# Kernel optimization log

Hardware: AMD Instinct MI355X
Metric: run time of the kernel (lower is better)

Reference implementation:

```python
import jax, jax.numpy as jnp
import numpy as np

N = 100000      # nodes
E = 1600000     # edges (avg degree 16)
H = 128         # hidden_dim
V = 64          # vector_dim
NUM_LAYERS = 3


def setup_inputs() -> dict:
    key = jax.random.key(0)
    ks = jax.random.split(key, 16)
    s = 0.05
    inp = {
        "node_feats": jax.random.normal(ks[0], (N, 1), dtype=jnp.float32),
        "edge_index": jax.random.randint(ks[1], (2, E), 0, N, dtype=jnp.int64),
        "batch": jnp.zeros((N,), dtype=jnp.int64),
        "temperature": jnp.float32(1.0),
        "t": jnp.float32(1.0),
        # SAGEConv layer 0: in=1 -> out=H. PyG: lin_l (on aggregated, with bias), lin_r (on root, no bias)
        "Wl0": jax.random.normal(ks[2], (1, H), dtype=jnp.float32) * s,
        "bl0": jnp.zeros((H,), dtype=jnp.float32),
        "Wr0": jax.random.normal(ks[3], (1, H), dtype=jnp.float32) * s,
        # SAGEConv layers 1..2: H -> H, stacked
        "Wl": jax.random.normal(ks[4], (NUM_LAYERS - 1, H, H), dtype=jnp.float32) * s,
        "bl": jnp.zeros((NUM_LAYERS - 1, H), dtype=jnp.float32),
        "Wr": jax.random.normal(ks[5], (NUM_LAYERS - 1, H, H), dtype=jnp.float32) * s,
        # to_vector: H -> V
        "Wv": jax.random.normal(ks[6], (H, V), dtype=jnp.float32) * s,
        "bv": jnp.zeros((V,), dtype=jnp.float32),
        # mlp: (V+2) -> H -> 1
        "Wm1": jax.random.normal(ks[7], (V + 2, H), dtype=jnp.float32) * s,
        "bm1": jnp.zeros((H,), dtype=jnp.float32),
        "Wm2": jax.random.normal(ks[8], (H, 1), dtype=jnp.float32) * s,
        "bm2": jnp.zeros((1,), dtype=jnp.float32),
    }
    return inp


def reference(node_feats, edge_index, batch, temperature, t,
              Wl0, bl0, Wr0, Wl, bl, Wr, Wv, bv, Wm1, bm1, Wm2, bm2):
    n = node_feats.shape[0]
    src, dst = edge_index[0], edge_index[1]
    # in-degree for scatter-mean (clamp to 1 for isolated nodes, like PyG mean aggr)
    deg = jax.ops.segment_sum(jnp.ones((src.shape[0],), node_feats.dtype), dst, num_segments=n)
    deg = jnp.maximum(deg, 1.0)[:, None]  # (N,1)

    def sage(h, Wl_, bl_, Wr_):
        # scatter-mean of source features onto destination nodes
        agg = jax.ops.segment_sum(h[src], dst, num_segments=n) / deg
        return agg @ Wl_ + bl_ + h @ Wr_

    h = node_feats.reshape(-1, 1)  # (N,1)
    h = jax.nn.relu(sage(h, Wl0, bl0, Wr0))
    for i in range(Wl.shape[0]):
        h = jax.nn.relu(sage(h, Wl[i], bl[i], Wr[i]))

    # global_mean_pool over single graph (batch all zeros)
    num_graphs = 1
    cnt = jax.ops.segment_sum(jnp.ones((n,), h.dtype), batch, num_segments=num_graphs)
    pooled = jax.ops.segment_sum(h, batch, num_segments=num_graphs) / jnp.maximum(cnt, 1.0)[:, None]  # (1,H)

    z = pooled @ Wv + bv  # (1,V)  (no ReLU in original code path)
    extras = jnp.stack([jnp.asarray(temperature, z.dtype), jnp.asarray(t, z.dtype)]).reshape(1, 2)
    feat = jnp.concatenate([z, extras], axis=1)  # (1, V+2)
    out = jax.nn.softplus(jax.nn.relu(feat @ Wm1 + bm1) @ Wm2 + bm2)  # (1,1)
    return out
```

## Files before the change

### kernel.cpp

```cpp
#include <hip/hip_runtime.h>
#include <hip/hip_bf16.h>
#include <math.h>

#define H 128
#define BKT_SHIFT 9
#define BKT_NODES 512
#define CHUNK 2048
#define GEMM_GRID 512
#define FP8_SCALE 64.0f
#define FP8_INV (1.0f / 64.0f)

typedef __attribute__((ext_vector_type(8))) short short8;
typedef __attribute__((ext_vector_type(4))) float f32x4;
typedef __attribute__((ext_vector_type(2))) float f32x2;

static __device__ __forceinline__ ushort f2b(float v) {
    union { float f; unsigned u; } x; x.f = v;
    unsigned r = x.u + 0x7fffu + ((x.u >> 16) & 1u);
    return (ushort)(r >> 16);
}
static __device__ __forceinline__ float b2f(ushort b) {
    union { unsigned u; float f; } x; x.u = ((unsigned)b) << 16;
    return x.f;
}


__global__ void bucket_hist_kernel(const int* __restrict__ dst, int e,
                                   int* __restrict__ bucketCount, int* __restrict__ blockBase) {
    __shared__ int hist[256];
    int t = threadIdx.x;
    hist[t] = 0;
    __syncthreads();
    int base = blockIdx.x * CHUNK;
    #pragma unroll
    for (int k = 0; k < CHUNK / 256; k++) {
        int i = base + k * 256 + t;
        if (i < e) atomicAdd(&hist[dst[i] >> BKT_SHIFT], 1);
    }
    __syncthreads();
    blockBase[blockIdx.x * 256 + t] = atomicAdd(&bucketCount[t], hist[t]);
}

__global__ void bucket_scan_kernel(const int* __restrict__ bucketCount, int* __restrict__ bucketBase,
                                   int* __restrict__ rs, int n, int e) {
    if (threadIdx.x == 0 && blockIdx.x == 0) {
        int acc = 0;
        for (int i = 0; i < 256; i++) { bucketBase[i] = acc; acc += bucketCount[i]; }
        bucketBase[256] = acc;
        rs[n] = e;
    }
}

__global__ void bucket_scatter_kernel(const int* __restrict__ src, const int* __restrict__ dst, int e,
                                      const int* __restrict__ bucketBase, const int* __restrict__ blockBase,
                                      int2* __restrict__ grouped) {
    __shared__ int cur[256];
    int t = threadIdx.x;
    cur[t] = bucketBase[t] + blockBase[blockIdx.x * 256 + t];
    __syncthreads();
    int base = blockIdx.x * CHUNK;
    #pragma unroll
    for (int k = 0; k < CHUNK / 256; k++) {
        int i = base + k * 256 + t;
        if (i < e) {
            int d = dst[i];
            int pos = atomicAdd(&cur[d >> BKT_SHIFT], 1);
            int2 p; p.x = d; p.y = src[i];
            grouped[pos] = p;
        }
    }
}

__global__ void bucket_csr_kernel(const int2* __restrict__ grouped, const int* __restrict__ bucketBase,
                                  int* __restrict__ rs, int* __restrict__ csr, int n) {
    __shared__ int sdeg[BKT_NODES];
    __shared__ int sexcl[BKT_NODES];
    __shared__ int wsum[4];
    int b = blockIdx.x;
    int t = threadIdx.x;
    int nodeBase = b << BKT_SHIFT;
    int ebase = bucketBase[b], eend = bucketBase[b + 1];
    sdeg[t] = 0; sdeg[t + 256] = 0;
    __syncthreads();
    for (int e = ebase + t; e < eend; e += 256)
        atomicAdd(&sdeg[grouped[e].x - nodeBase], 1);
    __syncthreads();
    int lane = t & 63, wid = t >> 6;
    int v0 = sdeg[2 * t], v1 = sdeg[2 * t + 1];
    int p = v0 + v1;
    int x = p;
    #pragma unroll
    for (int off = 1; off < 64; off <<= 1) {
        int y = __shfl_up(x, off, 64);
        if (lane >= off) x += y;
    }
    if (lane == 63) wsum[wid] = x;
    __syncthreads();
    if (t == 0) {
        int acc = 0;
        #pragma unroll
        for (int w = 0; w < 4; w++) { int tmp = wsum[w]; wsum[w] = acc; acc += tmp; }
    }
    __syncthreads();
    int basep = wsum[wid] + x - p;
    sexcl[2 * t] = basep;
    sexcl[2 * t + 1] = basep + v0;
    int nodes = min(BKT_NODES, n - nodeBase);
    for (int i = t; i < nodes; i += 256) rs[nodeBase + i] = ebase + sexcl[i];
    sdeg[t] = 0; sdeg[t + 256] = 0;
    __syncthreads();
    for (int e = ebase + t; e < eend; e += 256) {
        int2 pr = grouped[e];
        int l = pr.x - nodeBase;
        int r = atomicAdd(&sdeg[l], 1);
        csr[ebase + sexcl[l] + r] = pr.y;
    }
}


__global__ void prep_w_kernel(const float* __restrict__ Wl, const float* __restrict__ Wr,
                              ushort* __restrict__ Btg) {
    int idx = blockIdx.x * 256 + threadIdx.x;
    if (idx >= 65536) return;
    int l = idx >> 15;
    int col = (idx >> 8) & 127;
    int k = idx & 255;
    float v = (k < 128) ? Wl[l * H * H + k * H + col] : Wr[l * H * H + (k - 128) * H + col];
    Btg[idx] = f2b(v);
}


__global__ void agg0_kernel(const float* __restrict__ x, const int* __restrict__ rs,
                            const int* __restrict__ csr, float* __restrict__ agg0, int n) {
    int i = blockIdx.x * 256 + threadIdx.x;
    if (i >= n) return;
    int a = rs[i], b = rs[i + 1];
    float s = 0.f;
    for (int e = a; e < b; e++) s += x[csr[e]];
    agg0[i] = s / (float)max(b - a, 1);
}

__global__ void expand0_kernel(const float* __restrict__ x, const float* __restrict__ agg0,
                               const float* __restrict__ Wl0, const float* __restrict__ bl0,
                               const float* __restrict__ Wr0, ushort* __restrict__ hout,
                               ushort* __restrict__ h8, int n) {
    int idx = blockIdx.x * 256 + threadIdx.x;
    if (idx >= n * 64) return;
    int i = idx >> 6, j = (idx & 63) * 2;
    float gi = agg0[i], xi = x[i];
    float v0 = fmaxf(gi * Wl0[j] + bl0[j] + xi * Wr0[j], 0.f);
    float v1 = fmaxf(gi * Wl0[j + 1] + bl0[j + 1] + xi * Wr0[j + 1], 0.f);
    ushort2 o; o.x = f2b(v0); o.y = f2b(v1);
    *(ushort2*)(hout + (size_t)i * H + j) = o;
    int p = __builtin_amdgcn_cvt_pk_fp8_f32(v0 * FP8_SCALE, v1 * FP8_SCALE, 0, false);
    h8[(size_t)i * 64 + (idx & 63)] = (ushort)p;
}


__global__ void aggregate8_kernel(const unsigned char* __restrict__ h8, const int* __restrict__ rs,
                                  const int* __restrict__ csr, ushort* __restrict__ aggb, int n) {
    int tid = threadIdx.x;
    int w = (tid >> 5) & 1;
    int node = blockIdx.x * 8 + (tid >> 6) * 2 + w;
    if (node >= n) return;
    int sl = (tid >> 3) & 3;
    int fl = tid & 7;
    int a = rs[node], b = rs[node + 1];
    f32x2 s[8];
    #pragma unroll
    for (int j = 0; j < 8; j++) s[j] = (f32x2){0.f, 0.f};

    int e = a;
    for (; e + 8 <= b; e += 8) {
        int n0 = csr[e + sl], n1 = csr[e + 4 + sl];
        uint4 u0 = *(const uint4*)(h8 + (size_t)n0 * 128 + 16 * fl);
        uint4 u1 = *(const uint4*)(h8 + (size_t)n1 * 128 + 16 * fl);
        unsigned dw[8] = {u0.x, u0.y, u0.z, u0.w, u1.x, u1.y, u1.z, u1.w};
        #pragma unroll
        for (int d = 0; d < 8; d++) {
            f32x2 lo = __builtin_amdgcn_cvt_pk_f32_fp8(dw[d], false);
            f32x2 hi = __builtin_amdgcn_cvt_pk_f32_fp8(dw[d], true);
            s[(d & 3) * 2] += lo;
            s[(d & 3) * 2 + 1] += hi;
        }
    }
    for (; e + 4 <= b; e += 4) {
        int n0 = csr[e + sl];
        uint4 u0 = *(const uint4*)(h8 + (size_t)n0 * 128 + 16 * fl);
        unsigned dw[4] = {u0.x, u0.y, u0.z, u0.w};
        #pragma unroll
        for (int d = 0; d < 4; d++) {
            f32x2 lo = __builtin_amdgcn_cvt_pk_f32_fp8(dw[d], false);
            f32x2 hi = __builtin_amdgcn_cvt_pk_f32_fp8(dw[d], true);
            s[d * 2] += lo;
            s[d * 2 + 1] += hi;
        }
    }
    if (e < b && sl < (b - e)) {
        int n0 = csr[e + sl];
        uint4 u0 = *(const uint4*)(h8 + (size_t)n0 * 128 + 16 * fl);
        unsigned dw[4] = {u0.x, u0.y, u0.z, u0.w};
        #pragma unroll
        for (int d = 0; d < 4; d++) {
            f32x2 lo = __builtin_amdgcn_cvt_pk_f32_fp8(dw[d], false);
            f32x2 hi = __builtin_amdgcn_cvt_pk_f32_fp8(dw[d], true);
            s[d * 2] += lo;
            s[d * 2 + 1] += hi;
        }
    }
    #pragma unroll
    for (int j = 0; j < 8; j++) {
        s[j].x += __shfl_xor(s[j].x, 8, 64);
        s[j].y += __shfl_xor(s[j].y, 8, 64);
        s[j].x += __shfl_xor(s[j].x, 16, 64);
        s[j].y += __shfl_xor(s[j].y, 16, 64);
    }
    if (sl == 0) {
        float inv = FP8_INV / (float)max(b - a, 1);
        short8 o0, o1;
        #pragma unroll
        for (int j = 0; j < 4; j++) {
            o0[2 * j]     = (short)f2b(s[j].x * inv);
            o0[2 * j + 1] = (short)f2b(s[j].y * inv);
            o1[2 * j]     = (short)f2b(s[j + 4].x * inv);
            o1[2 * j + 1] = (short)f2b(s[j + 4].y * inv);
        }
        ushort* dstp = aggb + (size_t)node * H + 16 * fl;
        *(short8*)dstp = o0;
        *(short8*)(dstp + 8) = o1;
    }
}


template<bool POOL>
__global__ __launch_bounds__(256, 2) void gemm_kernel(
    const ushort* __restrict__ aggb, const ushort* __restrict__ hb,
    const ushort* __restrict__ Btg,
    const float* __restrict__ bias, ushort* __restrict__ out,
    unsigned char* __restrict__ out8,
    float* __restrict__ partial, int nblk, int n) {
    __shared__ float sums[2][128];
    int tid = threadIdx.x;
    int wave = tid >> 6, lane = tid & 63;
    int l15 = lane & 15, lhi = lane >> 4;
    int colhalf = wave & 1;
    int rowsub = wave >> 1;
    int colbase = colhalf * 64;

    short8 bf[4][8];
    #pragma unroll
    for (int c2 = 0; c2 < 4; c2++) {
        const ushort* wp = Btg + (colbase + c2 * 16 + l15) * 256 + lhi * 8;
        #pragma unroll
        for (int s = 0; s < 8; s++)
            bf[c2][s] = *(const short8*)(wp + s * 32);
    }
    f32x4 bias_v[4];
    #pragma unroll
    for (int c2 = 0; c2 < 4; c2++)
        bias_v[c2] = *(const f32x4*)(bias + colbase + c2 * 16 + lhi * 4);

    f32x4 fs[4];
    #pragma unroll
    for (int c2 = 0; c2 < 4; c2++) fs[c2] = (f32x4){0.f, 0.f, 0.f, 0.f};

    for (int r0 = blockIdx.x * 32; r0 < n; r0 += nblk * 32) {
        int row = r0 + rowsub * 16 + l15;
        int arow = min(row, n - 1);
        short8 af[8];
        #pragma unroll
        for (int s = 0; s < 8; s++)
            af[s] = *(const short8*)((s < 4 ? aggb : hb) + (size_t)arow * H + (s & 3) * 32 + lhi * 8);
        f32x4 acc[4];
        #pragma unroll
        for (int c2 = 0; c2 < 4; c2++) acc[c2] = (f32x4){0.f, 0.f, 0.f, 0.f};
        #pragma unroll
        for (int s = 0; s < 8; s++) {
            #pragma unroll
            for (int c2 = 0; c2 < 4; c2++)
                acc[c2] = __builtin_amdgcn_mfma_f32_16x16x32_bf16(bf[c2][s], af[s], acc[c2], 0, 0, 0);
        }
        if (row < n) {
            if (POOL) {
                #pragma unroll
                for (int c2 = 0; c2 < 4; c2++)
                    #pragma unroll
                    for (int r = 0; r < 4; r++)
                        fs[c2][r] += fmaxf(acc[c2][r] + bias_v[c2][r], 0.f);
            } else {
                #pragma unroll
                for (int c2 = 0; c2 < 4; c2++) {
                    float v0 = fmaxf(acc[c2][0] + bias_v[c2][0], 0.f);
                    float v1 = fmaxf(acc[c2][1] + bias_v[c2][1], 0.f);
                    float v2 = fmaxf(acc[c2][2] + bias_v[c2][2], 0.f);
                    float v3 = fmaxf(acc[c2][3] + bias_v[c2][3], 0.f);
                    ushort4 o;
                    o.x = f2b(v0); o.y = f2b(v1); o.z = f2b(v2); o.w = f2b(v3);
                    *(ushort4*)(out + (size_t)row * H + colbase + c2 * 16 + lhi * 4) = o;
                    int p = __builtin_amdgcn_cvt_pk_fp8_f32(v0 * FP8_SCALE, v1 * FP8_SCALE, 0, false);
                    p = __builtin_amdgcn_cvt_pk_fp8_f32(v2 * FP8_SCALE, v3 * FP8_SCALE, p, true);
                    *(unsigned int*)(out8 + (size_t)row * 128 + colbase + c2 * 16 + lhi * 4) = (unsigned)p;
                }
            }
        }
    }

    if (POOL) {
        #pragma unroll
        for (int c2 = 0; c2 < 4; c2++) {
            #pragma unroll
            for (int m = 1; m < 16; m <<= 1) {
                #pragma unroll
                for (int r = 0; r < 4; r++)
                    fs[c2][r] += __shfl_xor(fs[c2][r], m, 64);
            }
        }
        if (l15 == 0) {
            #pragma unroll
            for (int c2 = 0; c2 < 4; c2++)
                #pragma unroll
                for (int r = 0; r < 4; r++)
                    sums[rowsub][colbase + c2 * 16 + lhi * 4 + r] = fs[c2][r];
        }
        __syncthreads();
        if (tid < 128)
            partial[tid * nblk + blockIdx.x] = sums[0][tid] + sums[1][tid];
    }
}


__global__ void pool_reduce_kernel(const float* __restrict__ partial, float* __restrict__ pooled,
                                   int nb, float invn) {
    int j = blockIdx.x;
    int t = threadIdx.x;
    float s = 0.f;
    for (int b = t; b < nb; b += 64) s += partial[j * nb + b];
    #pragma unroll
    for (int off = 32; off > 0; off >>= 1) s += __shfl_down(s, off, 64);
    if (t == 0) pooled[j] = s * invn;
}


__global__ void mlp_kernel(const float* __restrict__ pooled,
                           const float* __restrict__ Wv, const float* __restrict__ bv,
                           const float* __restrict__ temp, const float* __restrict__ tt,
                           const float* __restrict__ Wm1, const float* __restrict__ bm1,
                           const float* __restrict__ Wm2, const float* __restrict__ bm2,
                           float* __restrict__ out) {
    __shared__ float feat[66];
    __shared__ float red[2];
    int j = threadIdx.x;
    if (j < 64) {
        float s = bv[j];
        for (int k = 0; k < H; k++) s += pooled[k] * Wv[k * 64 + j];
        feat[j] = s;
    }
    if (j == 64) feat[64] = temp[0];
    if (j == 65) feat[65] = tt[0];
    __syncthreads();
    float m = bm1[j];
    for (int k = 0; k < 66; k++) m += feat[k] * Wm1[k * H + j];
    m = fmaxf(m, 0.f);
    float p = m * Wm2[j];
    #pragma unroll
    for (int off = 32; off > 0; off >>= 1) p += __shfl_down(p, off, 64);
    if ((j & 63) == 0) red[j >> 6] = p;
    __syncthreads();
    if (j == 0) {
        float x = red[0] + red[1] + bm2[0];
        out[0] = (x > 20.f) ? x : log1pf(expf(x));
    }
}


extern "C" void kernel_launch(void* const* d_in, const int* in_sizes, int n_in,
                              void* d_out, int out_size, void* d_ws, size_t ws_size,
                              hipStream_t stream) {
    const float* node_feats = (const float*)d_in[0];
    const int* edge_index = (const int*)d_in[1];
    const float* temp = (const float*)d_in[3];
    const float* tt   = (const float*)d_in[4];
    const float* Wl0 = (const float*)d_in[5];
    const float* bl0 = (const float*)d_in[6];
    const float* Wr0 = (const float*)d_in[7];
    const float* Wl  = (const float*)d_in[8];
    const float* bl  = (const float*)d_in[9];
    const float* Wr  = (const float*)d_in[10];
    const float* Wv  = (const float*)d_in[11];
    const float* bv  = (const float*)d_in[12];
    const float* Wm1 = (const float*)d_in[13];
    const float* bm1 = (const float*)d_in[14];
    const float* Wm2 = (const float*)d_in[15];
    const float* bm2 = (const float*)d_in[16];

    const int N = in_sizes[0];
    const int E = in_sizes[1] / 2;
    const int* src = edge_index;
    const int* dst = edge_index + E;

    size_t NH = (size_t)N * H;
    ushort* hA   = (ushort*)d_ws;
    ushort* hB   = hA + NH;
    ushort* aggb = hB + NH;
    ushort* Btg  = aggb + NH;
    float* agg0  = (float*)(Btg + 65536);
    int2* grouped = (int2*)(agg0 + N);
    int* csr     = (int*)(grouped + E);
    int* rs      = csr + E;
    int* bucketCount = rs + (N + 1);
    int* bucketBase  = bucketCount + 256;
    int* blockBase   = bucketBase + 257;
    int NBLK = (E + CHUNK - 1) / CHUNK;
    float* partial = (float*)(blockBase + NBLK * 256);
    float* pooled  = partial + (size_t)H * GEMM_GRID;
    unsigned char* hB8 = (unsigned char*)(pooled + H);
    unsigned char* hA8 = (unsigned char*)grouped;

    int NB = (N + BKT_NODES - 1) / BKT_NODES;

    hipMemsetAsync(bucketCount, 0, 256 * sizeof(int), stream);
    bucket_hist_kernel<<<NBLK, 256, 0, stream>>>(dst, E, bucketCount, blockBase);
    bucket_scan_kernel<<<1, 64, 0, stream>>>(bucketCount, bucketBase, rs, N, E);
    bucket_scatter_kernel<<<NBLK, 256, 0, stream>>>(src, dst, E, bucketBase, blockBase, grouped);
    bucket_csr_kernel<<<NB, 256, 0, stream>>>(grouped, bucketBase, rs, csr, N);

    prep_w_kernel<<<256, 256, 0, stream>>>(Wl, Wr, Btg);

    agg0_kernel<<<(N + 255) / 256, 256, 0, stream>>>(node_feats, rs, csr, agg0, N);
    expand0_kernel<<<((size_t)N * 64 + 255) / 256, 256, 0, stream>>>(
        node_feats, agg0, Wl0, bl0, Wr0, hA, (ushort*)hA8, N);

    aggregate8_kernel<<<(N + 7) / 8, 256, 0, stream>>>(hA8, rs, csr, aggb, N);
    gemm_kernel<false><<<GEMM_GRID, 256, 0, stream>>>(aggb, hA, Btg, bl, hB, hB8, nullptr, GEMM_GRID, N);

    aggregate8_kernel<<<(N + 7) / 8, 256, 0, stream>>>(hB8, rs, csr, aggb, N);
    gemm_kernel<true><<<GEMM_GRID, 256, 0, stream>>>(aggb, hB, Btg + 32768, bl + H, nullptr, nullptr, partial, GEMM_GRID, N);

    pool_reduce_kernel<<<H, 64, 0, stream>>>(partial, pooled, GEMM_GRID, 1.0f / (float)N);
    mlp_kernel<<<1, H, 0, stream>>>(pooled, Wv, bv, temp, tt, Wm1, bm1, Wm2, bm2, (float*)d_out);
}
```

Measured before the change: 259.4 us.

## Drop bf16 node features, use fp8 root input in GEMM, fuse layer0 and pool/MLP

The bf16 copies of the hidden states are removed. The GEMM now reads the root features from the fp8 buffer, converts them to bf16 in registers, and folds the fp8 scale into Wr. Bucket scatter packs (src<<9 | local dst) into one 32-bit word instead of an int2, halving that traffic. agg0 and expand0 merge into a single layer0 kernel with vectorized fp8 stores, and pool_reduce plus mlp merge into one kernel. Root features now lose precision to fp8, and the packing assumes node indices fit in 23 bits.

```diff
diff --git a/kernel.cpp b/kernel.cpp
--- a/kernel.cpp
+++ b/kernel.cpp
@@ -19,10 +19,6 @@
     unsigned r = x.u + 0x7fffu + ((x.u >> 16) & 1u);
     return (ushort)(r >> 16);
 }
-static __device__ __forceinline__ float b2f(ushort b) {
-    union { unsigned u; float f; } x; x.u = ((unsigned)b) << 16;
-    return x.f;
-}
 
 
 __global__ void bucket_hist_kernel(const int* __restrict__ dst, int e,
@@ -53,7 +49,7 @@
 
 __global__ void bucket_scatter_kernel(const int* __restrict__ src, const int* __restrict__ dst, int e,
                                       const int* __restrict__ bucketBase, const int* __restrict__ blockBase,
-                                      int2* __restrict__ grouped) {
+                                      unsigned* __restrict__ grouped) {
     __shared__ int cur[256];
     int t = threadIdx.x;
     cur[t] = bucketBase[t] + blockBase[blockIdx.x * 256 + t];
@@ -65,13 +61,12 @@
         if (i < e) {
             int d = dst[i];
             int pos = atomicAdd(&cur[d >> BKT_SHIFT], 1);
-            int2 p; p.x = d; p.y = src[i];
-            grouped[pos] = p;
-        }
-    }
-}
-
-__global__ void bucket_csr_kernel(const int2* __restrict__ grouped, const int* __restrict__ bucketBase,
+            grouped[pos] = ((unsigned)src[i] << 9) | (unsigned)(d & 511);
+        }
+    }
+}
+
+__global__ void bucket_csr_kernel(const unsigned* __restrict__ grouped, const int* __restrict__ bucketBase,
                                   int* __restrict__ rs, int* __restrict__ csr, int n) {
     __shared__ int sdeg[BKT_NODES];
     __shared__ int sexcl[BKT_NODES];
@@ -83,7 +78,7 @@
     sdeg[t] = 0; sdeg[t + 256] = 0;
     __syncthreads();
     for (int e = ebase + t; e < eend; e += 256)
-        atomicAdd(&sdeg[grouped[e].x - nodeBase], 1);
+        atomicAdd(&sdeg[grouped[e] & 511u], 1);
     __syncthreads();
     int lane = t & 63, wid = t >> 6;
     int v0 = sdeg[2 * t], v1 = sdeg[2 * t + 1];
@@ -110,10 +105,10 @@
     sdeg[t] = 0; sdeg[t + 256] = 0;
     __syncthreads();
     for (int e = ebase + t; e < eend; e += 256) {
-        int2 pr = grouped[e];
-        int l = pr.x - nodeBase;
+        unsigned pr = grouped[e];
+        int l = (int)(pr & 511u);
         int r = atomicAdd(&sdeg[l], 1);
-        csr[ebase + sexcl[l] + r] = pr.y;
+        csr[ebase + sexcl[l] + r] = (int)(pr >> 9);
     }
 }
 
@@ -125,35 +120,57 @@
     int l = idx >> 15;
     int col = (idx >> 8) & 127;
     int k = idx & 255;
-    float v = (k < 128) ? Wl[l * H * H + k * H + col] : Wr[l * H * H + (k - 128) * H + col];
+    float v = (k < 128) ? Wl[l * H * H + k * H + col]
+                        : Wr[l * H * H + (k - 128) * H + col] * FP8_INV;
     Btg[idx] = f2b(v);
 }
 
 
-__global__ void agg0_kernel(const float* __restrict__ x, const int* __restrict__ rs,
-                            const int* __restrict__ csr, float* __restrict__ agg0, int n) {
-    int i = blockIdx.x * 256 + threadIdx.x;
-    if (i >= n) return;
-    int a = rs[i], b = rs[i + 1];
-    float s = 0.f;
-    for (int e = a; e < b; e++) s += x[csr[e]];
-    agg0[i] = s / (float)max(b - a, 1);
-}
-
-__global__ void expand0_kernel(const float* __restrict__ x, const float* __restrict__ agg0,
-                               const float* __restrict__ Wl0, const float* __restrict__ bl0,
-                               const float* __restrict__ Wr0, ushort* __restrict__ hout,
-                               ushort* __restrict__ h8, int n) {
-    int idx = blockIdx.x * 256 + threadIdx.x;
-    if (idx >= n * 64) return;
-    int i = idx >> 6, j = (idx & 63) * 2;
-    float gi = agg0[i], xi = x[i];
-    float v0 = fmaxf(gi * Wl0[j] + bl0[j] + xi * Wr0[j], 0.f);
-    float v1 = fmaxf(gi * Wl0[j + 1] + bl0[j + 1] + xi * Wr0[j + 1], 0.f);
-    ushort2 o; o.x = f2b(v0); o.y = f2b(v1);
-    *(ushort2*)(hout + (size_t)i * H + j) = o;
-    int p = __builtin_amdgcn_cvt_pk_fp8_f32(v0 * FP8_SCALE, v1 * FP8_SCALE, 0, false);
-    h8[(size_t)i * 64 + (idx & 63)] = (ushort)p;
+__global__ void layer0_kernel(const float* __restrict__ x, const int* __restrict__ rs,
+                              const int* __restrict__ csr,
+                              const float* __restrict__ Wl0, const float* __restrict__ bl0,
+                              const float* __restrict__ Wr0,
+                              unsigned char* __restrict__ h8, int n) {
+    __shared__ float sagg[256], sx[256];
+    int base = blockIdx.x * 256;
+    int t = threadIdx.x;
+    int node = base + t;
+    if (node < n) {
+        int a = rs[node], b = rs[node + 1];
+        float s = 0.f;
+        int e = a;
+        for (; e + 4 <= b; e += 4)
+            s += x[csr[e]] + x[csr[e + 1]] + x[csr[e + 2]] + x[csr[e + 3]];
+        for (; e < b; e++) s += x[csr[e]];
+        sagg[t] = s / (float)max(b - a, 1);
+        sx[t] = x[node];
+    }
+    __syncthreads();
+    int nodes = min(256, n - base);
+    #pragma unroll
+    for (int pass = 0; pass < 4; pass++) {
+        int nl = pass * 64 + (t >> 2);
+        int p = t & 3;
+        if (nl < nodes) {
+            float gi = sagg[nl], xi = sx[nl];
+            float v[32];
+            #pragma unroll
+            for (int k = 0; k < 32; k++) {
+                int f = p * 32 + k;
+                v[k] = fmaxf(gi * Wl0[f] + bl0[f] + xi * Wr0[f], 0.f) * FP8_SCALE;
+            }
+            unsigned up[8];
+            #pragma unroll
+            for (int d = 0; d < 8; d++) {
+                int pk = __builtin_amdgcn_cvt_pk_fp8_f32(v[4 * d], v[4 * d + 1], 0, false);
+                pk = __builtin_amdgcn_cvt_pk_fp8_f32(v[4 * d + 2], v[4 * d + 3], pk, true);
+                up[d] = (unsigned)pk;
+            }
+            unsigned char* dst8 = h8 + (size_t)(base + nl) * 128 + p * 32;
+            *(uint4*)dst8 = (uint4){up[0], up[1], up[2], up[3]};
+            *(uint4*)(dst8 + 16) = (uint4){up[4], up[5], up[6], up[7]};
+        }
+    }
 }
 
 
@@ -178,10 +195,8 @@
         unsigned dw[8] = {u0.x, u0.y, u0.z, u0.w, u1.x, u1.y, u1.z, u1.w};
         #pragma unroll
         for (int d = 0; d < 8; d++) {
-            f32x2 lo = __builtin_amdgcn_cvt_pk_f32_fp8(dw[d], false);
-            f32x2 hi = __builtin_amdgcn_cvt_pk_f32_fp8(dw[d], true);
-            s[(d & 3) * 2] += lo;
-            s[(d & 3) * 2 + 1] += hi;
+            s[(d & 3) * 2]     += __builtin_amdgcn_cvt_pk_f32_fp8(dw[d], false);
+            s[(d & 3) * 2 + 1] += __builtin_amdgcn_cvt_pk_f32_fp8(dw[d], true);
         }
     }
     for (; e + 4 <= b; e += 4) {
@@ -190,10 +205,8 @@
         unsigned dw[4] = {u0.x, u0.y, u0.z, u0.w};
         #pragma unroll
         for (int d = 0; d < 4; d++) {
-            f32x2 lo = __builtin_amdgcn_cvt_pk_f32_fp8(dw[d], false);
-            f32x2 hi = __builtin_amdgcn_cvt_pk_f32_fp8(dw[d], true);
-            s[d * 2] += lo;
-            s[d * 2 + 1] += hi;
+            s[d * 2]     += __builtin_amdgcn_cvt_pk_f32_fp8(dw[d], false);
+            s[d * 2 + 1] += __builtin_amdgcn_cvt_pk_f32_fp8(dw[d], true);
         }
     }
     if (e < b && sl < (b - e)) {
@@ -202,10 +215,8 @@
         unsigned dw[4] = {u0.x, u0.y, u0.z, u0.w};
         #pragma unroll
         for (int d = 0; d < 4; d++) {
-            f32x2 lo = __builtin_amdgcn_cvt_pk_f32_fp8(dw[d], false);
-            f32x2 hi = __builtin_amdgcn_cvt_pk_f32_fp8(dw[d], true);
-            s[d * 2] += lo;
-            s[d * 2 + 1] += hi;
+            s[d * 2]     += __builtin_amdgcn_cvt_pk_f32_fp8(dw[d], false);
+            s[d * 2 + 1] += __builtin_amdgcn_cvt_pk_f32_fp8(dw[d], true);
         }
     }
     #pragma unroll
@@ -234,9 +245,9 @@
 
 template<bool POOL>
 __global__ __launch_bounds__(256, 2) void gemm_kernel(
-    const ushort* __restrict__ aggb, const ushort* __restrict__ hb,
+    const ushort* __restrict__ aggb, const unsigned char* __restrict__ h8,
     const ushort* __restrict__ Btg,
-    const float* __restrict__ bias, ushort* __restrict__ out,
+    const float* __restrict__ bias,
     unsigned char* __restrict__ out8,
     float* __restrict__ partial, int nblk, int n) {
     __shared__ float sums[2][128];
@@ -269,8 +280,23 @@
         int arow = min(row, n - 1);
         short8 af[8];
         #pragma unroll
-        for (int s = 0; s < 8; s++)
-            af[s] = *(const short8*)((s < 4 ? aggb : hb) + (size_t)arow * H + (s & 3) * 32 + lhi * 8);
+        for (int s = 0; s < 4; s++)
+            af[s] = *(const short8*)(aggb + (size_t)arow * H + s * 32 + lhi * 8);
+        #pragma unroll
+        for (int s = 0; s < 4; s++) {
+            uint2 u = *(const uint2*)(h8 + (size_t)arow * 128 + s * 32 + lhi * 8);
+            f32x2 a0 = __builtin_amdgcn_cvt_pk_f32_fp8(u.x, false);
+            f32x2 a1 = __builtin_amdgcn_cvt_pk_f32_fp8(u.x, true);
+            f32x2 a2 = __builtin_amdgcn_cvt_pk_f32_fp8(u.y, false);
+            f32x2 a3 = __builtin_amdgcn_cvt_pk_f32_fp8(u.y, true);
+            unsigned d0 = __builtin_amdgcn_perm(__builtin_bit_cast(unsigned, a0.y), __builtin_bit_cast(unsigned, a0.x), 0x07060302u);
+            unsigned d1 = __builtin_amdgcn_perm(__builtin_bit_cast(unsigned, a1.y), __builtin_bit_cast(unsigned, a1.x), 0x07060302u);
+            unsigned d2 = __builtin_amdgcn_perm(__builtin_bit_cast(unsigned, a2.y), __builtin_bit_cast(unsigned, a2.x), 0x07060302u);
+            unsigned d3 = __builtin_amdgcn_perm(__builtin_bit_cast(unsigned, a3.y), __builtin_bit_cast(unsigned, a3.x), 0x07060302u);
+            union { unsigned u4[4]; short8 s8; } pk;
+            pk.u4[0] = d0; pk.u4[1] = d1; pk.u4[2] = d2; pk.u4[3] = d3;
+            af[4 + s] = pk.s8;
+        }
         f32x4 acc[4];
         #pragma unroll
         for (int c2 = 0; c2 < 4; c2++) acc[c2] = (f32x4){0.f, 0.f, 0.f, 0.f};
@@ -290,16 +316,13 @@
             } else {
                 #pragma unroll
                 for (int c2 = 0; c2 < 4; c2++) {
-                    float v0 = fmaxf(acc[c2][0] + bias_v[c2][0], 0.f);
-                    float v1 = fmaxf(acc[c2][1] + bias_v[c2][1], 0.f);
-                    float v2 = fmaxf(acc[c2][2] + bias_v[c2][2], 0.f);
-                    float v3 = fmaxf(acc[c2][3] + bias_v[c2][3], 0.f);
-                    ushort4 o;
-                    o.x = f2b(v0); o.y = f2b(v1); o.z = f2b(v2); o.w = f2b(v3);
-                    *(ushort4*)(out + (size_t)row * H + colbase + c2 * 16 + lhi * 4) = o;
-                    int p = __builtin_amdgcn_cvt_pk_fp8_f32(v0 * FP8_SCALE, v1 * FP8_SCALE, 0, false);
-                    p = __builtin_amdgcn_cvt_pk_fp8_f32(v2 * FP8_SCALE, v3 * FP8_SCALE, p, true);
-                    *(unsigned int*)(out8 + (size_t)row * 128 + colbase + c2 * 16 + lhi * 4) = (unsigned)p;
+                    float v0 = fmaxf(acc[c2][0] + bias_v[c2][0], 0.f) * FP8_SCALE;
+                    float v1 = fmaxf(acc[c2][1] + bias_v[c2][1], 0.f) * FP8_SCALE;
+                    float v2 = fmaxf(acc[c2][2] + bias_v[c2][2], 0.f) * FP8_SCALE;
+                    float v3 = fmaxf(acc[c2][3] + bias_v[c2][3], 0.f) * FP8_SCALE;
+                    int pk = __builtin_amdgcn_cvt_pk_fp8_f32(v0, v1, 0, false);
+                    pk = __builtin_amdgcn_cvt_pk_fp8_f32(v2, v3, pk, true);
+                    *(unsigned*)(out8 + (size_t)row * 128 + colbase + c2 * 16 + lhi * 4) = (unsigned)pk;
                 }
             }
         }
@@ -324,50 +347,51 @@
         }
         __syncthreads();
         if (tid < 128)
-            partial[tid * nblk + blockIdx.x] = sums[0][tid] + sums[1][tid];
-    }
-}
-
-
-__global__ void pool_reduce_kernel(const float* __restrict__ partial, float* __restrict__ pooled,
-                                   int nb, float invn) {
-    int j = blockIdx.x;
+            partial[(size_t)blockIdx.x * 128 + tid] = sums[0][tid] + sums[1][tid];
+    }
+}
+
+
+__global__ void pool_mlp_kernel(const float* __restrict__ partial, int nblk, float invn,
+                                const float* __restrict__ Wv, const float* __restrict__ bv,
+                                const float* __restrict__ temp, const float* __restrict__ tt,
+                                const float* __restrict__ Wm1, const float* __restrict__ bm1,
+                                const float* __restrict__ Wm2, const float* __restrict__ bm2,
+                                float* __restrict__ out) {
+    __shared__ float ps[256];
+    __shared__ float pooled[128];
+    __shared__ float feat[66];
+    __shared__ float red[4];
     int t = threadIdx.x;
+    int f = t & 127, hh = t >> 7;
     float s = 0.f;
-    for (int b = t; b < nb; b += 64) s += partial[j * nb + b];
-    #pragma unroll
-    for (int off = 32; off > 0; off >>= 1) s += __shfl_down(s, off, 64);
-    if (t == 0) pooled[j] = s * invn;
-}
-
-
-__global__ void mlp_kernel(const float* __restrict__ pooled,
-                           const float* __restrict__ Wv, const float* __restrict__ bv,
-                           const float* __restrict__ temp, const float* __restrict__ tt,
-                           const float* __restrict__ Wm1, const float* __restrict__ bm1,
-                           const float* __restrict__ Wm2, const float* __restrict__ bm2,
-                           float* __restrict__ out) {
-    __shared__ float feat[66];
-    __shared__ float red[2];
-    int j = threadIdx.x;
-    if (j < 64) {
-        float s = bv[j];
-        for (int k = 0; k < H; k++) s += pooled[k] * Wv[k * 64 + j];
-        feat[j] = s;
-    }
-    if (j == 64) feat[64] = temp[0];
-    if (j == 65) feat[65] = tt[0];
-    __syncthreads();
-    float m = bm1[j];
-    for (int k = 0; k < 66; k++) m += feat[k] * Wm1[k * H + j];
-    m = fmaxf(m, 0.f);
-    float p = m * Wm2[j];
+    int half = nblk >> 1;
+    for (int b = hh * half; b < (hh + 1) * half; b++) s += partial[(size_t)b * 128 + f];
+    ps[t] = s;
+    __syncthreads();
+    if (t < 128) pooled[t] = (ps[t] + ps[t + 128]) * invn;
+    __syncthreads();
+    if (t < 64) {
+        float z = bv[t];
+        for (int k = 0; k < H; k++) z += pooled[k] * Wv[k * 64 + t];
+        feat[t] = z;
+    }
+    if (t == 64) feat[64] = temp[0];
+    if (t == 65) feat[65] = tt[0];
+    __syncthreads();
+    float p = 0.f;
+    if (t < 128) {
+        float m = bm1[t];
+        for (int k = 0; k < 66; k++) m += feat[k] * Wm1[k * H + t];
+        m = fmaxf(m, 0.f);
+        p = m * Wm2[t];
+    }
     #pragma unroll
     for (int off = 32; off > 0; off >>= 1) p += __shfl_down(p, off, 64);
-    if ((j & 63) == 0) red[j >> 6] = p;
-    __syncthreads();
-    if (j == 0) {
-        float x = red[0] + red[1] + bm2[0];
+    if ((t & 63) == 0) red[t >> 6] = p;
+    __syncthreads();
+    if (t == 0) {
+        float x = red[0] + red[1] + red[2] + red[3] + bm2[0];
         out[0] = (x > 20.f) ? x : log1pf(expf(x));
     }
 }
@@ -399,12 +423,11 @@
     const int* dst = edge_index + E;
 
     size_t NH = (size_t)N * H;
-    ushort* hA   = (ushort*)d_ws;
-    ushort* hB   = hA + NH;
-    ushort* aggb = hB + NH;
+    ushort* aggb = (ushort*)d_ws;
     ushort* Btg  = aggb + NH;
-    float* agg0  = (float*)(Btg + 65536);
-    int2* grouped = (int2*)(agg0 + N);
+    unsigned char* hA8 = (unsigned char*)(Btg + 65536);
+    unsigned char* hB8 = hA8 + NH;
+    unsigned* grouped = (unsigned*)(hB8 + NH);
     int* csr     = (int*)(grouped + E);
     int* rs      = csr + E;
     int* bucketCount = rs + (N + 1);
@@ -412,9 +435,6 @@
     int* blockBase   = bucketBase + 257;
     int NBLK = (E + CHUNK - 1) / CHUNK;
     float* partial = (float*)(blockBase + NBLK * 256);
-    float* pooled  = partial + (size_t)H * GEMM_GRID;
-    unsigned char* hB8 = (unsigned char*)(pooled + H);
-    unsigned char* hA8 = (unsigned char*)grouped;
 
     int NB = (N + BKT_NODES - 1) / BKT_NODES;
 
@@ -426,16 +446,14 @@
 
     prep_w_kernel<<<256, 256, 0, stream>>>(Wl, Wr, Btg);
 
-    agg0_kernel<<<(N + 255) / 256, 256, 0, stream>>>(node_feats, rs, csr, agg0, N);
-    expand0_kernel<<<((size_t)N * 64 + 255) / 256, 256, 0, stream>>>(
-        node_feats, agg0, Wl0, bl0, Wr0, hA, (ushort*)hA8, N);
+    layer0_kernel<<<(N + 255) / 256, 256, 0, stream>>>(node_feats, rs, csr, Wl0, bl0, Wr0, hA8, N);
 
     aggregate8_kernel<<<(N + 7) / 8, 256, 0, stream>>>(hA8, rs, csr, aggb, N);
-    gemm_kernel<false><<<GEMM_GRID, 256, 0, stream>>>(aggb, hA, Btg, bl, hB, hB8, nullptr, GEMM_GRID, N);
+    gemm_kernel<false><<<GEMM_GRID, 256, 0, stream>>>(aggb, hA8, Btg, bl, hB8, nullptr, GEMM_GRID, N);
 
     aggregate8_kernel<<<(N + 7) / 8, 256, 0, stream>>>(hB8, rs, csr, aggb, N);
-    gemm_kernel<true><<<GEMM_GRID, 256, 0, stream>>>(aggb, hB, Btg + 32768, bl + H, nullptr, nullptr, partial, GEMM_GRID, N);
-
-    pool_reduce_kernel<<<H, 64, 0, stream>>>(partial, pooled, GEMM_GRID, 1.0f / (float)N);
-    mlp_kernel<<<1, H, 0, stream>>>(pooled, Wv, bv, temp, tt, Wm1, bm1, Wm2, bm2, (float*)d_out);
-}
+    gemm_kernel<true><<<GEMM_GRID, 256, 0, stream>>>(aggb, hB8, Btg + 32768, bl + H, nullptr, partial, GEMM_GRID, N);
+
+    pool_mlp_kernel<<<1, 256, 0, stream>>>(partial, GEMM_GRID, 1.0f / (float)N,
+                                           Wv, bv, temp, tt, Wm1, bm1, Wm2, bm2, (float*)d_out);
+}
```

Result: slower. 293.4 us (+13.1%).
